# Kernel optimization log

Measured on AMD Instinct MI355X. Metric: run time of the kernel, lower is better.

Reference implementation:

```python
import jax, jax.numpy as jnp
import numpy as np

HORIZON = 15
LAT = 6
CIN = 48  # input_dim // horizon
EPS = 1e-5
PAD = (HORIZON - 1) // 2  # 7


def _conv1d(x, w, b):
    # x: [B, Cin, L], w: [Cout, Cin, K], 'same' padding (pad=7, K=15)
    y = jax.lax.conv_general_dilated(
        x, w, window_strides=(1,), padding=[(PAD, PAD)],
        dimension_numbers=('NCH', 'OIH', 'NCH'))
    return y + b[None, :, None]


def _bn_ncl(x, g, b):
    # BatchNorm1d train-mode on [N, C, L]: stats over (N, L), biased var
    m = jnp.mean(x, axis=(0, 2), keepdims=True)
    v = jnp.mean(jnp.square(x - m), axis=(0, 2), keepdims=True)
    return (x - m) * jax.lax.rsqrt(v + EPS) * g[None, :, None] + b[None, :, None]


def setup_inputs() -> dict:
    key = jax.random.key(0)
    ks = jax.random.split(key, 16)
    B = 65536
    s1 = 1.0 / np.sqrt(CIN * HORIZON)
    s2 = 1.0 / np.sqrt(CIN * HORIZON)
    s3 = 1.0 / np.sqrt(2 * LAT * HORIZON)
    sp = 1.0 / np.sqrt(HORIZON)
    return {
        'x':  jax.random.normal(ks[0], (B, CIN * HORIZON), jnp.float32),
        'w1': jax.random.normal(ks[1], (CIN, CIN, HORIZON), jnp.float32) * s1,
        'b1': jax.random.normal(ks[2], (CIN,), jnp.float32) * s1,
        'g1': jnp.ones((CIN,), jnp.float32),
        'be1': jnp.zeros((CIN,), jnp.float32),
        'w2': jax.random.normal(ks[3], (2 * LAT, CIN, HORIZON), jnp.float32) * s2,
        'b2': jax.random.normal(ks[4], (2 * LAT,), jnp.float32) * s2,
        'g2': jnp.ones((2 * LAT,), jnp.float32),
        'be2': jnp.zeros((2 * LAT,), jnp.float32),
        'w3': jax.random.normal(ks[5], (LAT, 2 * LAT, HORIZON), jnp.float32) * s3,
        'b3': jax.random.normal(ks[6], (LAT,), jnp.float32) * s3,
        'pw': jax.random.normal(ks[7], (LAT, 2, HORIZON), jnp.float32) * sp,
        'pb': jax.random.normal(ks[8], (LAT, 2), jnp.float32) * sp,
        'pg': jnp.ones((LAT, 2), jnp.float32),
        'pbe': jnp.zeros((LAT, 2), jnp.float32),
    }


def reference(x, w1, b1, g1, be1, w2, b2, g2, be2, w3, b3, pw, pb, pg, pbe):
    B = x.shape[0]
    h = x.reshape(B, CIN, HORIZON)
    h = jax.nn.elu(_bn_ncl(_conv1d(h, w1, b1), g1, be1))
    h = jax.nn.elu(_bn_ncl(_conv1d(h, w2, b2), g2, be2))
    h = _conv1d(h, w3, b3)  # [B, LAT, HORIZON]

    # FFT spectral stats over last dim (length 15 -> 8 rfft bins)
    rf = jnp.fft.rfft(h, axis=2)
    power = jnp.square(jnp.abs(rf[:, :, 1:]))  # drop DC, [B, LAT, 7]
    freqs = jnp.arange(1, HORIZON // 2 + 1, dtype=h.dtype)  # rfftfreq(15)[1:]*15
    psum = jnp.sum(power, axis=2)
    f = jnp.sum(freqs * power, axis=2) / psum
    a = 2.0 * jnp.sqrt(psum) / HORIZON
    b_off = jnp.real(rf[:, :, 0]) / HORIZON

    # per-channel phase encoder, vectorized: Linear(15->2) + BatchNorm1d(2)
    v = jnp.einsum('bcl,col->bco', h, pw) + pb  # [B, LAT, 2]
    m = jnp.mean(v, axis=0, keepdims=True)
    var = jnp.mean(jnp.square(v - m), axis=0, keepdims=True)
    v = (v - m) * jax.lax.rsqrt(var + EPS) * pg + pbe
    p = jnp.arctan2(v[..., 1], v[..., 0]) / (2.0 * np.pi)  # [B, LAT]

    return jnp.concatenate([p, f, a, b_off], axis=-1)  # [B, 4*LAT]
```

## Files before the change

kernel.cpp:

```cpp
#include <hip/hip_runtime.h>
#include <math.h>

#define HORIZON 15
#define PAD 7
#define CIN 48
#define C2 12
#define LAT 6
#define EPS 1e-5f
#define NREP 16

typedef __bf16 bf16x8 __attribute__((ext_vector_type(8)));
typedef float f32x4 __attribute__((ext_vector_type(4)));
typedef unsigned short ushort8v __attribute__((ext_vector_type(8)));
typedef unsigned short ushortT;

__device__ inline void bfsplit(float v, ushortT& h, ushortT& l) {
    __bf16 bh = (__bf16)v;
    float fh = (float)bh;
    __bf16 bl = (__bf16)(v - fh);
    h = __builtin_bit_cast(ushortT, bh);
    l = __builtin_bit_cast(ushortT, bl);
}

__global__ void prep_kernel(const float* __restrict__ w1, const float* __restrict__ w2,
                            const float* __restrict__ w3,
                            ushortT* __restrict__ w1h, ushortT* __restrict__ w1l,
                            ushortT* __restrict__ w2h, ushortT* __restrict__ w2l,
                            float* __restrict__ w3t, float* __restrict__ trig) {
    int idx = blockIdx.x * blockDim.x + threadIdx.x;
    const int n1 = 768 * 736;
    const int n2 = 192 * 736;
    const int n3 = C2 * HORIZON * LAT;
    if (idx < n1) {
        int n = idx / 736, k = idx % 736;
        float v = 0.f;
        if (n < 720 && k < 720) {
            int l = n / 48, co = n % 48, ci = k / 15, t = k % 15;
            int d = t - l;
            if (d >= -PAD && d <= PAD) v = w1[(co * CIN + ci) * HORIZON + (d + PAD)];
        }
        ushortT h, lo; bfsplit(v, h, lo);
        w1h[idx] = h; w1l[idx] = lo;
    } else if (idx < n1 + n2) {
        int j = idx - n1;
        int n = j / 736, k = j % 736;
        float v = 0.f;
        if (n < 180 && k < 720) {
            int l = n / 12, co = n % 12, t = k / 48, ci = k % 48;
            int d = t - l;
            if (d >= -PAD && d <= PAD) v = w2[(co * CIN + ci) * HORIZON + (d + PAD)];
        }
        ushortT h, lo; bfsplit(v, h, lo);
        w2h[j] = h; w2l[j] = lo;
    } else if (idx < n1 + n2 + n3) {
        int j = idx - n1 - n2;
        int co = j % LAT; int r = j / LAT; int k = r % HORIZON; int ci = r / HORIZON;
        w3t[j] = w3[(co * C2 + ci) * HORIZON + k];
    } else if (idx < n1 + n2 + n3 + 7 * HORIZON) {
        int j = idx - (n1 + n2 + n3);
        int l = j % HORIZON; int f = j / HORIZON + 1;
        double ang = -2.0 * 3.14159265358979323846 * (double)(f * l) / 15.0;
        trig[j * 2]     = (float)cos(ang);
        trig[j * 2 + 1] = (float)sin(ang);
    }
}

template <int NFRAG, int CSTAT, bool FUSE_BN>
__global__ __launch_bounds__(256, 2)
void gemm_split(const float* __restrict__ A, int Ka,
                const ushortT* __restrict__ Bh, const ushortT* __restrict__ Bl,
                const float* __restrict__ bnp,
                float* __restrict__ Y, int ldy, int nreal,
                float* __restrict__ stats) {
    constexpr int NB = (NFRAG == 15) ? 16 : 12;
    __shared__ ushortT s_ah[8 * 512];
    __shared__ ushortT s_al[8 * 512];
    __shared__ ushortT s_bh[NB * 512];
    __shared__ ushortT s_bl[NB * 512];
    __shared__ float s_stats[2 * CSTAT];

    const int tid = threadIdx.x;
    const int w = tid >> 6, lane = tid & 63;
    const int lr = lane & 15, lq = lane >> 4;
    if (tid < 2 * CSTAT) s_stats[tid] = 0.f;

    const long m_base = (long)blockIdx.x * 128;
    const int n0 = blockIdx.y * (NFRAG * 16);

    f32x4 acc[2][NFRAG];
#pragma unroll
    for (int i = 0; i < 2; i++)
#pragma unroll
        for (int j = 0; j < NFRAG; j++) acc[i][j] = (f32x4){0.f, 0.f, 0.f, 0.f};

    const int KSTEPS = 736 / 32;
    for (int ks = 0; ks < KSTEPS; ks++) {
        const int k0 = ks * 32;
        __syncthreads();

#pragma unroll
        for (int j = 0; j < NB / 4; j++) {
            int nb = w * (NB / 4) + j;
            long grow = (long)(n0 + nb * 16 + lr) * 736 + k0 + lq * 8;
            ushort8v bvh = *(const ushort8v*)(Bh + grow);
            ushort8v bvl = *(const ushort8v*)(Bl + grow);
            *(ushort8v*)(s_bh + nb * 512 + lane * 8) = bvh;
            *(ushort8v*)(s_bl + nb * 512 + lane * 8) = bvl;
        }

#pragma unroll
        for (int j = 0; j < 2; j++) {
            int fb = w * 2 + j;
            long m = m_base + fb * 16 + lr;
            int k = k0 + lq * 8;
            ushort8v vh = (ushort8v)0, vl = (ushort8v)0;
            if (k < Ka) {
                const float4* p = (const float4*)(A + m * (long)Ka + k);
                float4 u0 = p[0], u1 = p[1];
                float f[8] = {u0.x, u0.y, u0.z, u0.w, u1.x, u1.y, u1.z, u1.w};
#pragma unroll
                for (int jj = 0; jj < 8; jj++) {
                    float v = f[jj];
                    if (FUSE_BN) {
                        int c = (k + jj) % 48;
                        float h = fmaf(v, bnp[c * 2], bnp[c * 2 + 1]);
                        v = h > 0.f ? h : expm1f(h);
                    }
                    ushortT hh, ll; bfsplit(v, hh, ll);
                    vh[jj] = hh; vl[jj] = ll;
                }
            }
            *(ushort8v*)(s_ah + fb * 512 + lane * 8) = vh;
            *(ushort8v*)(s_al + fb * 512 + lane * 8) = vl;
        }

        __syncthreads();

        bf16x8 ah[2], al[2];
#pragma unroll
        for (int fr = 0; fr < 2; fr++) {
            ah[fr] = *(const bf16x8*)(s_ah + (w * 2 + fr) * 512 + lane * 8);
            al[fr] = *(const bf16x8*)(s_al + (w * 2 + fr) * 512 + lane * 8);
        }
#pragma unroll
        for (int fc = 0; fc < NFRAG; fc++) {
            bf16x8 bhf = *(const bf16x8*)(s_bh + fc * 512 + lane * 8);
            bf16x8 blf = *(const bf16x8*)(s_bl + fc * 512 + lane * 8);
#pragma unroll
            for (int fr = 0; fr < 2; fr++) {
                acc[fr][fc] = __builtin_amdgcn_mfma_f32_16x16x32_bf16(ah[fr], bhf, acc[fr][fc], 0, 0, 0);
                acc[fr][fc] = __builtin_amdgcn_mfma_f32_16x16x32_bf16(al[fr], bhf, acc[fr][fc], 0, 0, 0);
                acc[fr][fc] = __builtin_amdgcn_mfma_f32_16x16x32_bf16(ah[fr], blf, acc[fr][fc], 0, 0, 0);
            }
        }
    }

    float ps[3] = {0.f, 0.f, 0.f}, qs[3] = {0.f, 0.f, 0.f};
#pragma unroll
    for (int fc = 0; fc < NFRAG; fc++) {
        int col = n0 + fc * 16 + lr;
        int j = fc % 3;
#pragma unroll
        for (int fr = 0; fr < 2; fr++) {
#pragma unroll
            for (int r = 0; r < 4; r++) {
                float v = acc[fr][fc][r];
                long row = m_base + w * 32 + fr * 16 + lq * 4 + r;
                if (col < nreal) Y[row * (long)ldy + col] = v;
                ps[j] += v;
                qs[j] = fmaf(v, v, qs[j]);
            }
        }
    }
#pragma unroll
    for (int j = 0; j < 3; j++) {
        int c = (lr + 16 * j) % CSTAT;
        atomicAdd(&s_stats[c], ps[j]);
        atomicAdd(&s_stats[CSTAT + c], qs[j]);
    }
    __syncthreads();
    if (tid < 2 * CSTAT)
        atomicAdd(&stats[(blockIdx.x & (NREP - 1)) * 2 * CSTAT + tid], s_stats[tid]);
}

__global__ void finalize_bn(const float* __restrict__ stats, const float* __restrict__ g,
                            const float* __restrict__ be, float* __restrict__ bn,
                            int C, float invN) {
    int c = threadIdx.x;
    if (c >= C) return;
    float s1 = 0.f, s2 = 0.f;
    for (int r = 0; r < NREP; r++) { s1 += stats[r * 2 * C + c]; s2 += stats[r * 2 * C + C + c]; }
    float m   = s1 * invN;
    float var = s2 * invN - m * m;
    float sc  = g[c] * rsqrtf(var + EPS);
    bn[c * 2]     = sc;
    bn[c * 2 + 1] = fmaf(-m, sc, be[c]);
}

__global__ __launch_bounds__(256) void tail_kernel(const float* __restrict__ h2,
                                                   const float* __restrict__ w3t,
                                                   const float* __restrict__ b3,
                                                   const float* __restrict__ pw,
                                                   const float* __restrict__ trig,
                                                   const float* __restrict__ bn2,
                                                   float* __restrict__ out,
                                                   float* __restrict__ vout,
                                                   float* __restrict__ stats) {
    __shared__ float s_sum[2 * LAT];
    __shared__ float s_sq[2 * LAT];
    int t = threadIdx.x;
    if (t < 2 * LAT) { s_sum[t] = 0.f; s_sq[t] = 0.f; }
    __syncthreads();

    int id = blockIdx.x * 256 + t;
    int co = id % LAT;
    long b = id / LAT;
    const float* xr = h2 + b * (long)(C2 * HORIZON);

    float acc[HORIZON];
#pragma unroll
    for (int l = 0; l < HORIZON; l++) acc[l] = b3[co];

    for (int ci = 0; ci < C2; ci++) {
        float sc = bn2[ci * 2], sh = bn2[ci * 2 + 1];
        float xv[HORIZON];
#pragma unroll
        for (int tt = 0; tt < HORIZON; tt++) {
            float h = fmaf(xr[tt * C2 + ci], sc, sh);
            xv[tt] = h > 0.f ? h : expm1f(h);
        }
        float wv[HORIZON];
#pragma unroll
        for (int k = 0; k < HORIZON; k++) wv[k] = w3t[(ci * HORIZON + k) * LAT + co];
#pragma unroll
        for (int tt = 0; tt < HORIZON; tt++) {
            const int lo = (tt - PAD) > 0 ? (tt - PAD) : 0;
            const int hi = (tt + PAD) < (HORIZON - 1) ? (tt + PAD) : (HORIZON - 1);
#pragma unroll
            for (int l = lo; l <= hi; l++)
                acc[l] = fmaf(xv[tt], wv[tt - l + PAD], acc[l]);
        }
    }

    float ssum = 0.f;
#pragma unroll
    for (int l = 0; l < HORIZON; l++) ssum += acc[l];
    float b_off = ssum * (1.f / 15.f);

    float psum = 0.f, fnum = 0.f;
#pragma unroll
    for (int j = 0; j < 7; j++) {
        float re = 0.f, im = 0.f;
#pragma unroll
        for (int l = 0; l < HORIZON; l++) {
            float c = trig[(j * HORIZON + l) * 2];
            float s = trig[(j * HORIZON + l) * 2 + 1];
            re = fmaf(acc[l], c, re);
            im = fmaf(acc[l], s, im);
        }
        float p = fmaf(re, re, im * im);
        psum += p;
        fnum = fmaf((float)(j + 1), p, fnum);
    }
    float f = fnum / psum;
    float a = 2.f * sqrtf(psum) * (1.f / 15.f);

    float* orow = out + b * 24;
    orow[6 + co]  = f;
    orow[12 + co] = a;
    orow[18 + co] = b_off;

    float v0 = 0.f, v1 = 0.f;
#pragma unroll
    for (int l = 0; l < HORIZON; l++) {
        v0 = fmaf(acc[l], pw[(co * 2 + 0) * HORIZON + l], v0);
        v1 = fmaf(acc[l], pw[(co * 2 + 1) * HORIZON + l], v1);
    }
    vout[b * 12 + co * 2]     = v0;
    vout[b * 12 + co * 2 + 1] = v1;
    atomicAdd(&s_sum[co * 2], v0);
    atomicAdd(&s_sq[co * 2], v0 * v0);
    atomicAdd(&s_sum[co * 2 + 1], v1);
    atomicAdd(&s_sq[co * 2 + 1], v1 * v1);

    __syncthreads();
    float* st = stats + (blockIdx.x & (NREP - 1)) * 2 * (2 * LAT);
    if (t < 2 * LAT) {
        atomicAdd(&st[t], s_sum[t]);
        atomicAdd(&st[2 * LAT + t], s_sq[t]);
    }
}

__global__ void phase_kernel(const float* __restrict__ v, const float* __restrict__ bnP,
                             float* __restrict__ out, long B) {
    long b = (long)blockIdx.x * 256 + threadIdx.x;
    if (b >= B) return;
#pragma unroll
    for (int co = 0; co < LAT; co++) {
        float v0 = v[b * 12 + co * 2];
        float v1 = v[b * 12 + co * 2 + 1];
        int c0 = co * 2, c1 = co * 2 + 1;
        v0 = fmaf(v0, bnP[c0 * 2], bnP[c0 * 2 + 1]);
        v1 = fmaf(v1, bnP[c1 * 2], bnP[c1 * 2 + 1]);
        out[b * 24 + co] = atan2f(v1, v0) * 0.15915494309189535f;
    }
}

extern "C" void kernel_launch(void* const* d_in, const int* in_sizes, int n_in,
                              void* d_out, int out_size, void* d_ws, size_t ws_size,
                              hipStream_t stream) {
    const float* x   = (const float*)d_in[0];
    const float* w1  = (const float*)d_in[1];
    const float* g1  = (const float*)d_in[3];
    const float* be1 = (const float*)d_in[4];
    const float* w2  = (const float*)d_in[5];
    const float* g2  = (const float*)d_in[7];
    const float* be2 = (const float*)d_in[8];
    const float* w3  = (const float*)d_in[9];
    const float* b3  = (const float*)d_in[10];
    const float* pw  = (const float*)d_in[11];
    const float* pg  = (const float*)d_in[13];
    const float* pbe = (const float*)d_in[14];
    float* out = (float*)d_out;

    long B = (long)in_sizes[0] / (CIN * HORIZON);

    ushortT* w1h = (ushortT*)d_ws;
    ushortT* w1l = w1h + 768 * 736;
    ushortT* w2h = w1l + 768 * 736;
    ushortT* w2l = w2h + 192 * 736;
    float* y1 = (float*)(w2l + 192 * 736);
    float* y2 = y1 + B * 720;
    float* vv = y2 + B * 180;
    float* stats1 = vv + B * 12;
    float* stats2 = stats1 + NREP * 96;
    float* statsP = stats2 + NREP * 24;
    float* bn1 = statsP + NREP * 24;
    float* bn2 = bn1 + 96;
    float* bnP = bn2 + 24;
    float* w3t = bnP + 24;
    float* trig = w3t + C2 * HORIZON * LAT;

    hipMemsetAsync(stats1, 0, NREP * (96 + 24 + 24) * sizeof(float), stream);

    const int prep_total = 768 * 736 + 192 * 736 + C2 * HORIZON * LAT + 7 * HORIZON;
    prep_kernel<<<(prep_total + 255) / 256, 256, 0, stream>>>(w1, w2, w3, w1h, w1l, w2h, w2l, w3t, trig);

    gemm_split<15, 48, false><<<dim3((int)(B / 128), 3), 256, 0, stream>>>(
        x, 720, w1h, w1l, nullptr, y1, 720, 720, stats1);
    finalize_bn<<<1, 64, 0, stream>>>(stats1, g1, be1, bn1, CIN, 1.f / (float)(B * HORIZON));

    gemm_split<12, 12, true><<<dim3((int)(B / 128), 1), 256, 0, stream>>>(
        y1, 720, w2h, w2l, bn1, y2, 180, 180, stats2);
    finalize_bn<<<1, 64, 0, stream>>>(stats2, g2, be2, bn2, C2, 1.f / (float)(B * HORIZON));

    tail_kernel<<<(int)(B * LAT / 256), 256, 0, stream>>>(y2, w3t, b3, pw, trig, bn2, out, vv, statsP);
    finalize_bn<<<1, 64, 0, stream>>>(statsP, pg, pbe, bnP, 2 * LAT, 1.f / (float)B);

    phase_kernel<<<(int)((B + 255) / 256), 256, 0, stream>>>(vv, bnP, out, B);
}
```

Before: 772.4 us.

## Load pre-swizzled weights directly into MFMA registers, drop LDS staging

Weights are pre-arranged by the prep kernel into MFMA fragment order, so each wave reads its B fragments straight from global memory into registers, and A fragments are built in registers without going through shared memory. This removes the LDS round trips and the two block barriers per K step. The BN2+ELU step moves out of the tail kernel's inner loop into a separate elementwise pass, and expm1f is replaced by __expf-1. In exchange, each wave now re-reads the weights from global memory or cache, there is one more kernel launch with an extra read and write of y2, and the cheaper ELU is slightly less accurate near zero.

```diff
diff --git a/kernel.cpp b/kernel.cpp
--- a/kernel.cpp
+++ b/kernel.cpp
@@ -8,6 +8,8 @@
 #define LAT 6
 #define EPS 1e-5f
 #define NREP 16
+#define KA 720
+#define KSTEPS 23
 
 typedef __bf16 bf16x8 __attribute__((ext_vector_type(8)));
 typedef float f32x4 __attribute__((ext_vector_type(4)));
@@ -22,42 +24,54 @@
     l = __builtin_bit_cast(ushortT, bl);
 }
 
+__device__ inline float fast_elu(float h) {
+    return h > 0.f ? h : __expf(h) - 1.f;
+}
+
+__device__ inline float w1_band(const float* __restrict__ w1, int n, int k) {
+    if (n >= 720 || k >= 720) return 0.f;
+    int l = n / 48, co = n % 48, ci = k / 15, t = k % 15;
+    int d = t - l;
+    return (d >= -PAD && d <= PAD) ? w1[(co * CIN + ci) * HORIZON + (d + PAD)] : 0.f;
+}
+__device__ inline float w2_band(const float* __restrict__ w2, int n, int k) {
+    if (n >= 180 || k >= 720) return 0.f;
+    int l = n / 12, co = n % 12, t = k / 48, ci = k % 48;
+    int d = t - l;
+    return (d >= -PAD && d <= PAD) ? w2[(co * CIN + ci) * HORIZON + (d + PAD)] : 0.f;
+}
+
+#define N1SW (48 * KSTEPS * 512)
+#define N2SW (12 * KSTEPS * 512)
+
 __global__ void prep_kernel(const float* __restrict__ w1, const float* __restrict__ w2,
                             const float* __restrict__ w3,
-                            ushortT* __restrict__ w1h, ushortT* __restrict__ w1l,
-                            ushortT* __restrict__ w2h, ushortT* __restrict__ w2l,
+                            ushortT* __restrict__ w1swh, ushortT* __restrict__ w1swl,
+                            ushortT* __restrict__ w2swh, ushortT* __restrict__ w2swl,
                             float* __restrict__ w3t, float* __restrict__ trig) {
     int idx = blockIdx.x * blockDim.x + threadIdx.x;
-    const int n1 = 768 * 736;
-    const int n2 = 192 * 736;
     const int n3 = C2 * HORIZON * LAT;
-    if (idx < n1) {
-        int n = idx / 736, k = idx % 736;
-        float v = 0.f;
-        if (n < 720 && k < 720) {
-            int l = n / 48, co = n % 48, ci = k / 15, t = k % 15;
-            int d = t - l;
-            if (d >= -PAD && d <= PAD) v = w1[(co * CIN + ci) * HORIZON + (d + PAD)];
-        }
-        ushortT h, lo; bfsplit(v, h, lo);
-        w1h[idx] = h; w1l[idx] = lo;
-    } else if (idx < n1 + n2) {
-        int j = idx - n1;
-        int n = j / 736, k = j % 736;
-        float v = 0.f;
-        if (n < 180 && k < 720) {
-            int l = n / 12, co = n % 12, t = k / 48, ci = k % 48;
-            int d = t - l;
-            if (d >= -PAD && d <= PAD) v = w2[(co * CIN + ci) * HORIZON + (d + PAD)];
-        }
-        ushortT h, lo; bfsplit(v, h, lo);
-        w2h[j] = h; w2l[j] = lo;
-    } else if (idx < n1 + n2 + n3) {
-        int j = idx - n1 - n2;
+    if (idx < N1SW) {
+        int j = idx & 7, lane = (idx >> 3) & 63;
+        int ks = (idx >> 9) % KSTEPS, nb = idx / (KSTEPS * 512);
+        int n = nb * 16 + (lane & 15);
+        int k = ks * 32 + (lane >> 4) * 8 + j;
+        ushortT h, lo; bfsplit(w1_band(w1, n, k), h, lo);
+        w1swh[idx] = h; w1swl[idx] = lo;
+    } else if (idx < N1SW + N2SW) {
+        int e = idx - N1SW;
+        int j = e & 7, lane = (e >> 3) & 63;
+        int ks = (e >> 9) % KSTEPS, nb = e / (KSTEPS * 512);
+        int n = nb * 16 + (lane & 15);
+        int k = ks * 32 + (lane >> 4) * 8 + j;
+        ushortT h, lo; bfsplit(w2_band(w2, n, k), h, lo);
+        w2swh[e] = h; w2swl[e] = lo;
+    } else if (idx < N1SW + N2SW + n3) {
+        int j = idx - N1SW - N2SW;
         int co = j % LAT; int r = j / LAT; int k = r % HORIZON; int ci = r / HORIZON;
         w3t[j] = w3[(co * C2 + ci) * HORIZON + k];
-    } else if (idx < n1 + n2 + n3 + 7 * HORIZON) {
-        int j = idx - (n1 + n2 + n3);
+    } else if (idx < N1SW + N2SW + n3 + 7 * HORIZON) {
+        int j = idx - (N1SW + N2SW + n3);
         int l = j % HORIZON; int f = j / HORIZON + 1;
         double ang = -2.0 * 3.14159265358979323846 * (double)(f * l) / 15.0;
         trig[j * 2]     = (float)cos(ang);
@@ -67,25 +81,21 @@
 
 template <int NFRAG, int CSTAT, bool FUSE_BN>
 __global__ __launch_bounds__(256, 2)
-void gemm_split(const float* __restrict__ A, int Ka,
-                const ushortT* __restrict__ Bh, const ushortT* __restrict__ Bl,
-                const float* __restrict__ bnp,
-                float* __restrict__ Y, int ldy, int nreal,
-                float* __restrict__ stats) {
-    constexpr int NB = (NFRAG == 15) ? 16 : 12;
-    __shared__ ushortT s_ah[8 * 512];
-    __shared__ ushortT s_al[8 * 512];
-    __shared__ ushortT s_bh[NB * 512];
-    __shared__ ushortT s_bl[NB * 512];
+void gemm_direct(const float* __restrict__ A,
+                 const ushortT* __restrict__ Bh, const ushortT* __restrict__ Bl,
+                 const float* __restrict__ bnp,
+                 float* __restrict__ Y, int ldy, int nreal,
+                 float* __restrict__ stats) {
     __shared__ float s_stats[2 * CSTAT];
-
     const int tid = threadIdx.x;
     const int w = tid >> 6, lane = tid & 63;
     const int lr = lane & 15, lq = lane >> 4;
     if (tid < 2 * CSTAT) s_stats[tid] = 0.f;
-
-    const long m_base = (long)blockIdx.x * 128;
-    const int n0 = blockIdx.y * (NFRAG * 16);
+    __syncthreads();
+
+    const long m_base = (long)blockIdx.x * 128 + w * 32;
+    const int fg0 = blockIdx.y * NFRAG;
+    const int n0 = fg0 * 16;
 
     f32x4 acc[2][NFRAG];
 #pragma unroll
@@ -93,59 +103,40 @@
 #pragma unroll
         for (int j = 0; j < NFRAG; j++) acc[i][j] = (f32x4){0.f, 0.f, 0.f, 0.f};
 
-    const int KSTEPS = 736 / 32;
     for (int ks = 0; ks < KSTEPS; ks++) {
         const int k0 = ks * 32;
-        __syncthreads();
-
-#pragma unroll
-        for (int j = 0; j < NB / 4; j++) {
-            int nb = w * (NB / 4) + j;
-            long grow = (long)(n0 + nb * 16 + lr) * 736 + k0 + lq * 8;
-            ushort8v bvh = *(const ushort8v*)(Bh + grow);
-            ushort8v bvl = *(const ushort8v*)(Bl + grow);
-            *(ushort8v*)(s_bh + nb * 512 + lane * 8) = bvh;
-            *(ushort8v*)(s_bl + nb * 512 + lane * 8) = bvl;
-        }
-
-#pragma unroll
-        for (int j = 0; j < 2; j++) {
-            int fb = w * 2 + j;
-            long m = m_base + fb * 16 + lr;
-            int k = k0 + lq * 8;
+        const int kq = k0 + lq * 8;
+        const bool kv = kq < KA;
+
+        bf16x8 ah[2], al[2];
+#pragma unroll
+        for (int fr = 0; fr < 2; fr++) {
             ushort8v vh = (ushort8v)0, vl = (ushort8v)0;
-            if (k < Ka) {
-                const float4* p = (const float4*)(A + m * (long)Ka + k);
+            if (kv) {
+                const float4* p = (const float4*)(A + (m_base + fr * 16 + lr) * (long)KA + kq);
                 float4 u0 = p[0], u1 = p[1];
                 float f[8] = {u0.x, u0.y, u0.z, u0.w, u1.x, u1.y, u1.z, u1.w};
+                if (FUSE_BN) {
+                    int cb = kq % 48;
+#pragma unroll
+                    for (int jj = 0; jj < 8; jj++)
+                        f[jj] = fast_elu(fmaf(f[jj], bnp[(cb + jj) * 2], bnp[(cb + jj) * 2 + 1]));
+                }
 #pragma unroll
                 for (int jj = 0; jj < 8; jj++) {
-                    float v = f[jj];
-                    if (FUSE_BN) {
-                        int c = (k + jj) % 48;
-                        float h = fmaf(v, bnp[c * 2], bnp[c * 2 + 1]);
-                        v = h > 0.f ? h : expm1f(h);
-                    }
-                    ushortT hh, ll; bfsplit(v, hh, ll);
+                    ushortT hh, ll; bfsplit(f[jj], hh, ll);
                     vh[jj] = hh; vl[jj] = ll;
                 }
             }
-            *(ushort8v*)(s_ah + fb * 512 + lane * 8) = vh;
-            *(ushort8v*)(s_al + fb * 512 + lane * 8) = vl;
-        }
-
-        __syncthreads();
-
-        bf16x8 ah[2], al[2];
-#pragma unroll
-        for (int fr = 0; fr < 2; fr++) {
-            ah[fr] = *(const bf16x8*)(s_ah + (w * 2 + fr) * 512 + lane * 8);
-            al[fr] = *(const bf16x8*)(s_al + (w * 2 + fr) * 512 + lane * 8);
-        }
+            ah[fr] = __builtin_bit_cast(bf16x8, vh);
+            al[fr] = __builtin_bit_cast(bf16x8, vl);
+        }
+
 #pragma unroll
         for (int fc = 0; fc < NFRAG; fc++) {
-            bf16x8 bhf = *(const bf16x8*)(s_bh + fc * 512 + lane * 8);
-            bf16x8 blf = *(const bf16x8*)(s_bl + fc * 512 + lane * 8);
+            const long boff = ((long)(fg0 + fc) * KSTEPS + ks) * 512 + lane * 8;
+            bf16x8 bhf = *(const bf16x8*)(Bh + boff);
+            bf16x8 blf = *(const bf16x8*)(Bl + boff);
 #pragma unroll
             for (int fr = 0; fr < 2; fr++) {
                 acc[fr][fc] = __builtin_amdgcn_mfma_f32_16x16x32_bf16(ah[fr], bhf, acc[fr][fc], 0, 0, 0);
@@ -165,7 +156,7 @@
 #pragma unroll
             for (int r = 0; r < 4; r++) {
                 float v = acc[fr][fc][r];
-                long row = m_base + w * 32 + fr * 16 + lq * 4 + r;
+                long row = m_base + fr * 16 + lq * 4 + r;
                 if (col < nreal) Y[row * (long)ldy + col] = v;
                 ps[j] += v;
                 qs[j] = fmaf(v, v, qs[j]);
@@ -197,12 +188,23 @@
     bn[c * 2 + 1] = fmaf(-m, sc, be[c]);
 }
 
+__global__ void bn_act_kernel(float* __restrict__ y, const float* __restrict__ bn, long n4) {
+    long i = (long)blockIdx.x * 256 + threadIdx.x;
+    if (i >= n4) return;
+    float4 v = ((float4*)y)[i];
+    int c0 = (int)((i * 4) % 12);
+    v.x = fast_elu(fmaf(v.x, bn[c0 * 2],       bn[c0 * 2 + 1]));
+    v.y = fast_elu(fmaf(v.y, bn[(c0 + 1) * 2], bn[(c0 + 1) * 2 + 1]));
+    v.z = fast_elu(fmaf(v.z, bn[(c0 + 2) * 2], bn[(c0 + 2) * 2 + 1]));
+    v.w = fast_elu(fmaf(v.w, bn[(c0 + 3) * 2], bn[(c0 + 3) * 2 + 1]));
+    ((float4*)y)[i] = v;
+}
+
 __global__ __launch_bounds__(256) void tail_kernel(const float* __restrict__ h2,
                                                    const float* __restrict__ w3t,
                                                    const float* __restrict__ b3,
                                                    const float* __restrict__ pw,
                                                    const float* __restrict__ trig,
-                                                   const float* __restrict__ bn2,
                                                    float* __restrict__ out,
                                                    float* __restrict__ vout,
                                                    float* __restrict__ stats) {
@@ -222,13 +224,9 @@
     for (int l = 0; l < HORIZON; l++) acc[l] = b3[co];
 
     for (int ci = 0; ci < C2; ci++) {
-        float sc = bn2[ci * 2], sh = bn2[ci * 2 + 1];
         float xv[HORIZON];
 #pragma unroll
-        for (int tt = 0; tt < HORIZON; tt++) {
-            float h = fmaf(xr[tt * C2 + ci], sc, sh);
-            xv[tt] = h > 0.f ? h : expm1f(h);
-        }
+        for (int tt = 0; tt < HORIZON; tt++) xv[tt] = xr[tt * C2 + ci];
         float wv[HORIZON];
 #pragma unroll
         for (int k = 0; k < HORIZON; k++) wv[k] = w3t[(ci * HORIZON + k) * LAT + co];
@@ -325,11 +323,11 @@
 
     long B = (long)in_sizes[0] / (CIN * HORIZON);
 
-    ushortT* w1h = (ushortT*)d_ws;
-    ushortT* w1l = w1h + 768 * 736;
-    ushortT* w2h = w1l + 768 * 736;
-    ushortT* w2l = w2h + 192 * 736;
-    float* y1 = (float*)(w2l + 192 * 736);
+    ushortT* w1swh = (ushortT*)d_ws;
+    ushortT* w1swl = w1swh + N1SW;
+    ushortT* w2swh = w1swl + N1SW;
+    ushortT* w2swl = w2swh + N2SW;
+    float* y1 = (float*)(w2swl + N2SW);
     float* y2 = y1 + B * 720;
     float* vv = y2 + B * 180;
     float* stats1 = vv + B * 12;
@@ -343,18 +341,20 @@
 
     hipMemsetAsync(stats1, 0, NREP * (96 + 24 + 24) * sizeof(float), stream);
 
-    const int prep_total = 768 * 736 + 192 * 736 + C2 * HORIZON * LAT + 7 * HORIZON;
-    prep_kernel<<<(prep_total + 255) / 256, 256, 0, stream>>>(w1, w2, w3, w1h, w1l, w2h, w2l, w3t, trig);
-
-    gemm_split<15, 48, false><<<dim3((int)(B / 128), 3), 256, 0, stream>>>(
-        x, 720, w1h, w1l, nullptr, y1, 720, 720, stats1);
+    const int prep_total = N1SW + N2SW + C2 * HORIZON * LAT + 7 * HORIZON;
+    prep_kernel<<<(prep_total + 255) / 256, 256, 0, stream>>>(
+        w1, w2, w3, w1swh, w1swl, w2swh, w2swl, w3t, trig);
+
+    gemm_direct<15, 48, false><<<dim3((int)(B / 128), 3), 256, 0, stream>>>(
+        x, w1swh, w1swl, nullptr, y1, 720, 720, stats1);
     finalize_bn<<<1, 64, 0, stream>>>(stats1, g1, be1, bn1, CIN, 1.f / (float)(B * HORIZON));
 
-    gemm_split<12, 12, true><<<dim3((int)(B / 128), 1), 256, 0, stream>>>(
-        y1, 720, w2h, w2l, bn1, y2, 180, 180, stats2);
+    gemm_direct<12, 12, true><<<dim3((int)(B / 128), 1), 256, 0, stream>>>(
+        y1, w2swh, w2swl, bn1, y2, 180, 180, stats2);
     finalize_bn<<<1, 64, 0, stream>>>(stats2, g2, be2, bn2, C2, 1.f / (float)(B * HORIZON));
 
-    tail_kernel<<<(int)(B * LAT / 256), 256, 0, stream>>>(y2, w3t, b3, pw, trig, bn2, out, vv, statsP);
+    bn_act_kernel<<<(int)(B * 180 / 4 / 256), 256, 0, stream>>>(y2, bn2, B * 180 / 4);
+    tail_kernel<<<(int)(B * LAT / 256), 256, 0, stream>>>(y2, w3t, b3, pw, trig, out, vv, statsP);
     finalize_bn<<<1, 64, 0, stream>>>(statsP, pg, pbe, bnP, 2 * LAT, 1.f / (float)B);
 
     phase_kernel<<<(int)((B + 255) / 256), 256, 0, stream>>>(vv, bnP, out, B);
```

Measured after the change: 1.069 ms. +38.4%, slower.
